# Kernel optimization log

Measured on AMD Instinct MI355X. Metric: run time of the kernel, lower is better.

## Reference

```python
import jax, jax.numpy as jnp
import numpy as np

N_GRAPHS = 16
NODES_PER = 420
N = N_GRAPHS * NODES_PER      # 6720 nodes
DEG = 8
E = N * DEG                   # 53760 edges
HEADS = 2
IN_DIM = 2048
H1 = 1024                     # conv1 out per head
H2 = 64                       # conv2 out (heads=1)
OUT_DIM = 18
SCALE = 0.02


def _lin(x, W, b):
    return x @ W + b


def _transformer_conv(x, src, dst, Wq, bq, Wk, bk, Wv, bv, Ws, bs, heads, d):
    # PyG TransformerConv: per-edge dot-product attention, softmax over incoming
    # edges of each destination node, scatter-sum of messages, + root skip.
    n = x.shape[0]
    q = _lin(x, Wq, bq).reshape(n, heads, d)
    k = _lin(x, Wk, bk).reshape(n, heads, d)
    v = _lin(x, Wv, bv).reshape(n, heads, d)
    alpha = (q[dst] * k[src]).sum(-1) / jnp.sqrt(jnp.asarray(d, x.dtype))  # [E, heads]
    amax = jax.ops.segment_max(alpha, dst, num_segments=n)
    ex = jnp.exp(alpha - amax[dst])
    denom = jax.ops.segment_sum(ex, dst, num_segments=n)
    a = ex / (denom[dst] + 1e-16)
    out = jax.ops.segment_sum(v[src] * a[..., None], dst, num_segments=n)  # [N, heads, d]
    return out.reshape(n, heads * d) + _lin(x, Ws, bs)


def setup_inputs() -> dict:
    key = jax.random.key(0)
    ks = jax.random.split(key, 32)
    x = jax.random.normal(ks[0], (N, IN_DIM), dtype=jnp.float32)
    dst = jax.random.randint(ks[1], (E,), 0, N)
    # keep edges within each 420-node graph
    src = (dst // NODES_PER) * NODES_PER + jax.random.randint(ks[2], (E,), 0, NODES_PER)
    edge_index = jnp.stack([src, dst]).astype(jnp.int64)  # [2, E]
    connectivity = jax.random.randint(ks[3], (N,), 1, 6).astype(jnp.int64)  # lobes 1..5
    p = lambda i, shape: SCALE * jax.random.normal(ks[i], shape, dtype=jnp.float32)
    inp = {
        'x': x, 'edge_index': edge_index, 'connectivity': connectivity,
        'node_pe': p(4, (NODES_PER, IN_DIM)),
        'lobe_pe': p(5, (5, IN_DIM)),
        'lung_pe': p(6, (2, IN_DIM)),
        'Wq1': p(7, (IN_DIM, HEADS * H1)), 'bq1': jnp.zeros((HEADS * H1,), jnp.float32),
        'Wk1': p(8, (IN_DIM, HEADS * H1)), 'bk1': jnp.zeros((HEADS * H1,), jnp.float32),
        'Wv1': p(9, (IN_DIM, HEADS * H1)), 'bv1': jnp.zeros((HEADS * H1,), jnp.float32),
        'Ws1': p(10, (IN_DIM, HEADS * H1)), 'bs1': jnp.zeros((HEADS * H1,), jnp.float32),
        'Wq2': p(11, (HEADS * H1, H2)), 'bq2': jnp.zeros((H2,), jnp.float32),
        'Wk2': p(12, (HEADS * H1, H2)), 'bk2': jnp.zeros((H2,), jnp.float32),
        'Wv2': p(13, (HEADS * H1, H2)), 'bv2': jnp.zeros((H2,), jnp.float32),
        'Ws2': p(14, (HEADS * H1, H2)), 'bs2': jnp.zeros((H2,), jnp.float32),
        'W_fc1': p(15, (NODES_PER * H2, 256)), 'b_fc1': jnp.zeros((256,), jnp.float32),
        'W_fc2': p(16, (256, 128)), 'b_fc2': jnp.zeros((128,), jnp.float32),
        'W_fc3': p(17, (128, 64)), 'b_fc3': jnp.zeros((64,), jnp.float32),
        'W_fc4': p(18, (64, OUT_DIM)), 'b_fc4': jnp.zeros((OUT_DIM,), jnp.float32),
    }
    return inp


def reference(x, edge_index, connectivity, node_pe, lobe_pe, lung_pe,
              Wq1, bq1, Wk1, bk1, Wv1, bv1, Ws1, bs1,
              Wq2, bq2, Wk2, bk2, Wv2, bv2, Ws2, bs2,
              W_fc1, b_fc1, W_fc2, b_fc2, W_fc3, b_fc3, W_fc4, b_fc4):
    src, dst = edge_index[0], edge_index[1]
    # positional embeddings: node PE tiled per graph, lobe PE (conn in 1..5),
    # lung PE (lobes 1,2 -> lung 0; lobes 3,4,5 -> lung 1)
    h = x + jnp.tile(node_pe, (N_GRAPHS, 1))
    h = h + lobe_pe[connectivity - 1]
    h = h + lung_pe[jnp.where(connectivity <= 2, 0, 1)]
    h = jax.nn.relu(_transformer_conv(h, src, dst, Wq1, bq1, Wk1, bk1, Wv1, bv1, Ws1, bs1, HEADS, H1))
    h = jax.nn.relu(_transformer_conv(h, src, dst, Wq2, bq2, Wk2, bk2, Wv2, bv2, Ws2, bs2, 1, H2))
    h = h.reshape(-1, NODES_PER * H2)  # [B, 420*64]
    h = jax.nn.relu(_lin(h, W_fc1, b_fc1))
    h = jax.nn.relu(_lin(h, W_fc2, b_fc2))
    h = jax.nn.relu(_lin(h, W_fc3, b_fc3))
    return _lin(h, W_fc4, b_fc4)
```

## Files before the change

kernel.cpp:

```cpp
#include <hip/hip_runtime.h>
#include <stdint.h>

#define N_GRAPHS 16
#define NODES_PER 420
#define NN (N_GRAPHS * NODES_PER)
#define MP 6784
#define EE (NN * 8)
#define IN_DIM 2048
#define NCAT1 8192
#define NCAT2 256
#define KDIM 2048

typedef __bf16 bf16x8 __attribute__((ext_vector_type(8)));
typedef float f32x4 __attribute__((ext_vector_type(4)));
typedef unsigned short u16x8 __attribute__((ext_vector_type(8)));

__device__ __forceinline__ unsigned short f2bf(float f) {
  unsigned u = __float_as_uint(f);
  u += 0x7FFFu + ((u >> 16) & 1u);
  return (unsigned short)(u >> 16);
}
__device__ __forceinline__ float bf2f(unsigned short h) {
  return __uint_as_float(((unsigned)h) << 16);
}

__device__ __forceinline__ void gl2lds16(const void* g, const void* l) {
  __builtin_amdgcn_global_load_lds(
      (const __attribute__((address_space(1))) void*)(uintptr_t)g,
      (__attribute__((address_space(3))) void*)(unsigned int)(uintptr_t)l,
      16, 0, 0);
}

__global__ void prep_k(int* cnt, float* bcat1, float* f1,
                       const float* bq1, const float* bk1, const float* bv1, const float* bs1,
                       const float* bfc1) {
  int i = blockIdx.x * 256 + threadIdx.x;
  if (i < NN) cnt[i] = 0;
  if (i < NCAT1) {
    const float* p = i < 2048 ? bq1 : i < 4096 ? bk1 : i < 6144 ? bv1 : bs1;
    bcat1[i] = p[i & 2047];
  }
  if (i < 16 * 256) f1[i] = bfc1[i & 255];
}

__global__ void cnt_edges_k(const int* __restrict__ ei, int* __restrict__ cnt) {
  int e = blockIdx.x * 256 + threadIdx.x;
  if (e < EE) atomicAdd(&cnt[ei[EE + e]], 1);
}

__global__ __launch_bounds__(64) void scan_offs_k(const int* __restrict__ cnt,
                                                  int* __restrict__ offs,
                                                  int* __restrict__ cursor) {
  const int t = threadIdx.x;
  const int base = t * 105;
  int s = 0;
#pragma unroll 1
  for (int j = 0; j < 105; j++) s += cnt[base + j];
  int pfx = s;
#pragma unroll
  for (int d = 1; d < 64; d <<= 1) {
    int v = __shfl_up(pfx, d, 64);
    if (t >= d) pfx += v;
  }
  int run = pfx - s;
#pragma unroll 1
  for (int j = 0; j < 105; j++) {
    int idx = base + j;
    offs[idx] = run; cursor[idx] = run; run += cnt[idx];
  }
  if (t == 63) offs[NN] = run;
}

__global__ void scatter_k(const int* __restrict__ ei, int* __restrict__ cursor,
                          int* __restrict__ psrc) {
  int e = blockIdx.x * 256 + threadIdx.x;
  if (e < EE) {
    int d = ei[EE + e];
    int pos = atomicAdd(&cursor[d], 1);
    psrc[pos] = ei[e];
  }
}

__global__ void pe_add_k(const float* __restrict__ x, const int* __restrict__ conn,
                         const float* __restrict__ npe, const float* __restrict__ lpe,
                         const float* __restrict__ gpe, unsigned short* __restrict__ h0,
                         float* __restrict__ qkvs2,
                         const float* __restrict__ bq2, const float* __restrict__ bk2,
                         const float* __restrict__ bv2, const float* __restrict__ bs2) {
  const int n = blockIdx.x, t = threadIdx.x;
  const int c = conn[n];
  const float4* x4 = (const float4*)(x + (size_t)n * IN_DIM);
  const float4* n4 = (const float4*)(npe + (size_t)(n % NODES_PER) * IN_DIM);
  const float4* l4 = (const float4*)(lpe + (size_t)(c - 1) * IN_DIM);
  const float4* g4 = (const float4*)(gpe + (size_t)(c <= 2 ? 0 : 1) * IN_DIM);
  ushort4* o4 = (ushort4*)(h0 + (size_t)n * IN_DIM);
#pragma unroll
  for (int i = 0; i < 2; i++) {
    int idx = i * 256 + t;
    float4 a = x4[idx], b = n4[idx], cc = l4[idx], d = g4[idx];
    ushort4 o;
    o.x = f2bf(a.x + b.x + cc.x + d.x);
    o.y = f2bf(a.y + b.y + cc.y + d.y);
    o.z = f2bf(a.z + b.z + cc.z + d.z);
    o.w = f2bf(a.w + b.w + cc.w + d.w);
    o4[idx] = o;
  }
  const float* bp = t < 64 ? bq2 : t < 128 ? bk2 : t < 192 ? bv2 : bs2;
  qkvs2[(size_t)n * NCAT2 + t] = bp[t & 63];
}

__global__ void transw_k(const float* Wq1, const float* Wk1, const float* Wv1, const float* Ws1,
                         const float* Wq2, const float* Wk2, const float* Wv2, const float* Ws2,
                         unsigned short* __restrict__ o1, unsigned short* __restrict__ o2) {
  __shared__ float tile[32][33];
  const int z = blockIdx.z;
  const float* W;
  unsigned short* o;
  int n0, Ncol;
  const int k0 = blockIdx.y * 32;
  if (z < 4) {
    W = z == 0 ? Wq1 : z == 1 ? Wk1 : z == 2 ? Wv1 : Ws1;
    o = o1 + (size_t)z * 2048 * KDIM;
    n0 = blockIdx.x * 32; Ncol = 2048;
  } else {
    if (blockIdx.x >= 8) return;
    const int m = blockIdx.x >> 1;
    W = m == 0 ? Wq2 : m == 1 ? Wk2 : m == 2 ? Wv2 : Ws2;
    o = o2 + (size_t)m * 64 * KDIM;
    n0 = (blockIdx.x & 1) * 32; Ncol = 64;
  }
  const int tx = threadIdx.x, ty = threadIdx.y;
#pragma unroll
  for (int r = 0; r < 4; r++)
    tile[ty + r * 8][tx] = W[(size_t)(k0 + ty + r * 8) * Ncol + n0 + tx];
  __syncthreads();
#pragma unroll
  for (int r = 0; r < 4; r++)
    o[(size_t)(n0 + ty + r * 8) * KDIM + k0 + tx] = f2bf(tile[tx][ty + r * 8]);
}

template <int BM, int BN, int OUTF>
__launch_bounds__(256, 3)
__global__ void gemm_bt_k(const unsigned short* __restrict__ A,
                          const unsigned short* __restrict__ Bt,
                          const float* __restrict__ bias, void* __restrict__ C,
                          int Nsz, int K, int kIters) {
  constexpr int BK = 64;
  constexpr int WTM = BM / 32, WTN = BN / 32;
  constexpr int RA = BM / 32, RB = BN / 32;
  __shared__ __align__(16) unsigned short lA[BM * BK];
  __shared__ __align__(16) unsigned short lB[BN * BK];
  const int t = threadIdx.x;
  const int w = t >> 6, lane = t & 63;
  const int wm = w >> 1, wn = w & 1;
  const int quad = lane >> 4, l16 = lane & 15;
  const int m0 = blockIdx.y * BM, n0 = blockIdx.x * BN;

  f32x4 acc[WTM][WTN];
#pragma unroll
  for (int i = 0; i < WTM; i++)
#pragma unroll
    for (int j = 0; j < WTN; j++)
#pragma unroll
      for (int r = 0; r < 4; r++) acc[i][j][r] = 0.f;

  const int srow = t >> 3;
  const int scol = ((t & 7) ^ (srow & 7)) * 8;
  const unsigned short* Ab = A + (size_t)(m0 + srow) * K + scol + blockIdx.z * (size_t)kIters * BK;
  const unsigned short* Bb = Bt + (size_t)(n0 + srow) * K + scol + blockIdx.z * (size_t)kIters * BK;

  for (int it = 0; it < kIters; it++) {
    const int k0 = it * BK;
    __syncthreads();
#pragma unroll
    for (int r = 0; r < RA; r++)
      gl2lds16(Ab + (size_t)r * 32 * K + k0, (const char*)lA + r * 4096 + t * 16);
#pragma unroll
    for (int r = 0; r < RB; r++)
      gl2lds16(Bb + (size_t)r * 32 * K + k0, (const char*)lB + r * 4096 + t * 16);
    __syncthreads();

#pragma unroll
    for (int s = 0; s < 2; s++) {
      bf16x8 afr[WTM], bfr[WTN];
#pragma unroll
      for (int i = 0; i < WTM; i++) {
        int row = wm * (BM / 2) + i * 16 + l16;
        int slot = (s * 4 + quad) ^ (row & 7);
        afr[i] = __builtin_bit_cast(bf16x8, *(const int4*)(&lA[row * 64 + slot * 8]));
      }
#pragma unroll
      for (int j = 0; j < WTN; j++) {
        int row = wn * (BN / 2) + j * 16 + l16;
        int slot = (s * 4 + quad) ^ (row & 7);
        bfr[j] = __builtin_bit_cast(bf16x8, *(const int4*)(&lB[row * 64 + slot * 8]));
      }
#pragma unroll
      for (int i = 0; i < WTM; i++)
#pragma unroll
        for (int j = 0; j < WTN; j++)
          acc[i][j] = __builtin_amdgcn_mfma_f32_16x16x32_bf16(afr[i], bfr[j], acc[i][j], 0, 0, 0);
    }
  }

#pragma unroll
  for (int j = 0; j < WTN; j++) {
    const int col = n0 + wn * (BN / 2) + j * 16 + l16;
    const float bs = OUTF ? 0.f : bias[col];
#pragma unroll
    for (int i = 0; i < WTM; i++) {
#pragma unroll
      for (int r = 0; r < 4; r++) {
        int row = m0 + wm * (BM / 2) + i * 16 + quad * 4 + r;
        if constexpr (OUTF)
          atomicAdd(&((float*)C)[(size_t)row * Nsz + col], acc[i][j][r]);
        else
          ((unsigned short*)C)[(size_t)row * Nsz + col] = f2bf(acc[i][j][r] + bs);
      }
    }
  }
}

__global__ __launch_bounds__(256) void attn1_k(const unsigned short* __restrict__ qkvs,
                                               const int* __restrict__ offs,
                                               const int* __restrict__ psrc,
                                               unsigned short* __restrict__ h1) {
  const int bid = blockIdx.x;
  const int xcd = bid & 7, idx = bid >> 3;
  const int head = idx / 840;
  const int r2 = idx - head * 840;
  const int g = xcd * 2 + r2 / 420;
  const int n = g * 420 + r2 % 420;
  const int t = threadIdx.x, w = t >> 6, lane = t & 63;
  __shared__ __align__(16) unsigned short s_q[1024];
  __shared__ float s_al[64];
  __shared__ int s_src[64];
  __shared__ float s_m, s_l, s_sc;
  const size_t base = (size_t)n * NCAT1;
  const size_t ho = (size_t)head * 1024;
  *(ushort4*)(s_q + t * 4) = *(const ushort4*)(qkvs + base + ho + t * 4);
  float acc[4] = {0.f, 0.f, 0.f, 0.f};
  if (t == 0) { s_m = -1e30f; s_l = 0.f; }
  __syncthreads();
  const int e0 = offs[n], e1 = offs[n + 1];
  for (int c0 = e0; c0 < e1; c0 += 64) {
    const int ce = min(64, e1 - c0);
    if (t < ce) s_src[t] = psrc[c0 + t];
    __syncthreads();
    for (int e = w; e < ce; e += 4) {
      const unsigned short* kp = qkvs + (size_t)s_src[e] * NCAT1 + 2048 + ho;
      float p = 0.f;
#pragma unroll
      for (int i = 0; i < 2; i++) {
        u16x8 kv = *(const u16x8*)(kp + i * 512 + lane * 8);
        u16x8 qv = *(const u16x8*)(s_q + i * 512 + lane * 8);
#pragma unroll
        for (int j = 0; j < 8; j++) p += bf2f(qv[j]) * bf2f(kv[j]);
      }
#pragma unroll
      for (int s = 32; s > 0; s >>= 1) p += __shfl_xor(p, s, 64);
      if (lane == 0) s_al[e] = p * 0.03125f;
    }
    __syncthreads();
    if (t == 0) {
      float mo = s_m, mn = mo;
      for (int e = 0; e < ce; e++) mn = fmaxf(mn, s_al[e]);
      float sc = __expf(mo - mn);
      float l = s_l * sc;
      for (int e = 0; e < ce; e++) {
        float we = __expf(s_al[e] - mn);
        l += we;
        s_al[e] = we;
      }
      s_m = mn; s_l = l; s_sc = sc;
    }
    __syncthreads();
    const float sc = s_sc;
#pragma unroll
    for (int j = 0; j < 4; j++) acc[j] *= sc;
    for (int e = 0; e < ce; e++) {
      const unsigned short* vp = qkvs + (size_t)s_src[e] * NCAT1 + 4096 + ho;
      const float we = s_al[e];
      ushort4 vv = *(const ushort4*)(vp + t * 4);
      acc[0] += we * bf2f(vv.x);
      acc[1] += we * bf2f(vv.y);
      acc[2] += we * bf2f(vv.z);
      acc[3] += we * bf2f(vv.w);
    }
    __syncthreads();
  }
  const float inv = 1.f / (s_l + 1e-16f);
  ushort4 sk = *(const ushort4*)(qkvs + base + 6144 + ho + t * 4);
  ushort4 o;
  o.x = f2bf(fmaxf(acc[0] * inv + bf2f(sk.x), 0.f));
  o.y = f2bf(fmaxf(acc[1] * inv + bf2f(sk.y), 0.f));
  o.z = f2bf(fmaxf(acc[2] * inv + bf2f(sk.z), 0.f));
  o.w = f2bf(fmaxf(acc[3] * inv + bf2f(sk.w), 0.f));
  *(ushort4*)(h1 + (size_t)n * 2048 + ho + t * 4) = o;
}

__global__ __launch_bounds__(64) void attn2_k(const float* __restrict__ qkvs2,
                                              const int* __restrict__ offs,
                                              const int* __restrict__ psrc,
                                              float* __restrict__ h2) {
  const int bid = blockIdx.x;
  const int xcd = bid & 7, idx = bid >> 3;
  const int g = xcd * 2 + idx / 420;
  const int n = g * 420 + idx % 420;
  const int t = threadIdx.x;
  const size_t rb = (size_t)n * NCAT2;
  const float q = qkvs2[rb + t];
  float m = -1e30f, l = 0.f, acc = 0.f;
  const int e0 = offs[n], e1 = offs[n + 1];
  for (int e = e0; e < e1; e++) {
    const int src = psrc[e];
    float p = q * qkvs2[(size_t)src * NCAT2 + 64 + t];
#pragma unroll
    for (int s = 32; s > 0; s >>= 1) p += __shfl_xor(p, s, 64);
    p *= 0.125f;
    const float mn = fmaxf(m, p);
    const float sc = __expf(m - mn), we = __expf(p - mn);
    const float v = qkvs2[(size_t)src * NCAT2 + 128 + t];
    l = l * sc + we;
    acc = acc * sc + we * v;
    m = mn;
  }
  float o = acc / (l + 1e-16f) + qkvs2[rb + 192 + t];
  h2[(size_t)n * 64 + t] = fmaxf(o, 0.f);
}

__global__ __launch_bounds__(256) void fc1_k(const float* __restrict__ h2,
                                             const float* __restrict__ W,
                                             float* __restrict__ f1) {
  __shared__ float sA[16][256];
  const int t = threadIdx.x, k0 = blockIdx.x * 256;
#pragma unroll
  for (int r = 0; r < 16; r++) sA[r][t] = h2[(size_t)r * 26880 + k0 + t];
  __syncthreads();
  float acc[16];
#pragma unroll
  for (int r = 0; r < 16; r++) acc[r] = 0.f;
  for (int kk = 0; kk < 256; kk++) {
    const float wv = W[(size_t)(k0 + kk) * 256 + t];
#pragma unroll
    for (int r = 0; r < 16; r++) acc[r] += sA[r][kk] * wv;
  }
#pragma unroll
  for (int r = 0; r < 16; r++) atomicAdd(&f1[r * 256 + t], acc[r]);
}

__global__ __launch_bounds__(128) void fc234_k(const float* __restrict__ f1,
                                               const float* __restrict__ W2, const float* __restrict__ b2,
                                               const float* __restrict__ W3, const float* __restrict__ b3,
                                               const float* __restrict__ W4, const float* __restrict__ b4,
                                               float* __restrict__ out) {
  const int row = blockIdx.x, t = threadIdx.x;
  __shared__ float s2[128], s3[64];
  float acc = 0.f;
  for (int k = 0; k < 256; k++) acc += fmaxf(f1[row * 256 + k], 0.f) * W2[k * 128 + t];
  s2[t] = fmaxf(acc + b2[t], 0.f);
  __syncthreads();
  if (t < 64) {
    float a3 = 0.f;
    for (int k = 0; k < 128; k++) a3 += s2[k] * W3[k * 64 + t];
    s3[t] = fmaxf(a3 + b3[t], 0.f);
  }
  __syncthreads();
  if (t < 18) {
    float a4 = 0.f;
    for (int k = 0; k < 64; k++) a4 += s3[k] * W4[k * 18 + t];
    out[row * 18 + t] = a4 + b4[t];
  }
}

extern "C" void kernel_launch(void* const* d_in, const int* in_sizes, int n_in,
                              void* d_out, int out_size, void* d_ws, size_t ws_size,
                              hipStream_t stream) {
  const float* x    = (const float*)d_in[0];
  const int*   ei   = (const int*)d_in[1];
  const int*   conn = (const int*)d_in[2];
  const float* npe  = (const float*)d_in[3];
  const float* lpe  = (const float*)d_in[4];
  const float* gpe  = (const float*)d_in[5];
  const float* Wq1 = (const float*)d_in[6];  const float* bq1 = (const float*)d_in[7];
  const float* Wk1 = (const float*)d_in[8];  const float* bk1 = (const float*)d_in[9];
  const float* Wv1 = (const float*)d_in[10]; const float* bv1 = (const float*)d_in[11];
  const float* Ws1 = (const float*)d_in[12]; const float* bs1 = (const float*)d_in[13];
  const float* Wq2 = (const float*)d_in[14]; const float* bq2 = (const float*)d_in[15];
  const float* Wk2 = (const float*)d_in[16]; const float* bk2 = (const float*)d_in[17];
  const float* Wv2 = (const float*)d_in[18]; const float* bv2 = (const float*)d_in[19];
  const float* Ws2 = (const float*)d_in[20]; const float* bs2 = (const float*)d_in[21];
  const float* Wf1 = (const float*)d_in[22]; const float* bf1 = (const float*)d_in[23];
  const float* Wf2 = (const float*)d_in[24]; const float* bf2 = (const float*)d_in[25];
  const float* Wf3 = (const float*)d_in[26]; const float* bf3 = (const float*)d_in[27];
  const float* Wf4 = (const float*)d_in[28]; const float* bf4 = (const float*)d_in[29];
  float* out = (float*)d_out;

  char* ws = (char*)d_ws;
  size_t off = 0;
  auto alloc = [&](size_t bytes) -> void* {
    void* p = ws + off;
    off += (bytes + 255) & ~(size_t)255;
    return p;
  };
  unsigned short* h0    = (unsigned short*)alloc((size_t)MP * IN_DIM * 2);
  unsigned short* w1t   = (unsigned short*)alloc((size_t)NCAT1 * KDIM * 2);
  unsigned short* qkvs1 = (unsigned short*)alloc((size_t)MP * NCAT1 * 2);
  unsigned short* w2t   = (unsigned short*)alloc((size_t)NCAT2 * KDIM * 2);
  float* qkvs2 = (float*)alloc((size_t)MP * NCAT2 * 4);
  float* h2    = (float*)alloc((size_t)NN * 64 * 4);
  float* bcat1 = (float*)alloc(NCAT1 * 4);
  float* f1    = (float*)alloc(16 * 256 * 4);
  int* cnt    = (int*)alloc(NN * 4);
  int* offs   = (int*)alloc((NN + 1) * 4);
  int* cursor = (int*)alloc(NN * 4);
  int* psrc   = (int*)alloc(EE * 4);
  unsigned short* h1 = w1t;

  prep_k<<<32, 256, 0, stream>>>(cnt, bcat1, f1, bq1, bk1, bv1, bs1, bf1);
  cnt_edges_k<<<EE / 256, 256, 0, stream>>>(ei, cnt);
  scan_offs_k<<<1, 64, 0, stream>>>(cnt, offs, cursor);
  scatter_k<<<EE / 256, 256, 0, stream>>>(ei, cursor, psrc);
  pe_add_k<<<NN, 256, 0, stream>>>(x, conn, npe, lpe, gpe, h0, qkvs2,
                                   bq2, bk2, bv2, bs2);
  transw_k<<<dim3(64, 64, 5), dim3(32, 8), 0, stream>>>(
      Wq1, Wk1, Wv1, Ws1, Wq2, Wk2, Wv2, Ws2, w1t, w2t);
  gemm_bt_k<128, 128, 0><<<dim3(NCAT1 / 128, MP / 128, 1), 256, 0, stream>>>(
      h0, w1t, bcat1, qkvs1, NCAT1, KDIM, KDIM / 64);
  attn1_k<<<2 * NN, 256, 0, stream>>>(qkvs1, offs, psrc, h1);
  gemm_bt_k<64, 64, 1><<<dim3(NCAT2 / 64, MP / 64, 4), 256, 0, stream>>>(
      h1, w2t, nullptr, qkvs2, NCAT2, KDIM, KDIM / 64 / 4);
  attn2_k<<<NN, 64, 0, stream>>>(qkvs2, offs, psrc, h2);
  fc1_k<<<26880 / 256, 256, 0, stream>>>(h2, Wf1, f1);
  fc234_k<<<16, 128, 0, stream>>>(f1, Wf2, bf2, Wf3, bf3, Wf4, bf4, out);
}
```

Baseline: 613.9 us.

## Replace split-K atomics with partial buffers plus combine, parallelize scan, tweak GEMM occupancy

The conv2 split-K GEMM now writes each K-slice to its own partial buffer, reusing h0, with nontemporal stores instead of float atomicAdd. A new combine kernel sums the four slices and adds the conv2 bias, which moves out of pe_add_k into prep_k. The single-block offset scan widens from 64 to 256 threads with register caching and a cross-wave prefix, and the GEMM launch bounds ask for 4 blocks per SM instead of 3. This removes atomic contention at the cost of an extra kernel launch and more memory traffic, and the higher occupancy target may force register spills in the large GEMM.

```diff
diff --git a/kernel.cpp b/kernel.cpp
--- a/kernel.cpp
+++ b/kernel.cpp
@@ -31,8 +31,9 @@
       16, 0, 0);
 }
 
-__global__ void prep_k(int* cnt, float* bcat1, float* f1,
+__global__ void prep_k(int* cnt, float* bcat1, float* bcat2, float* f1,
                        const float* bq1, const float* bk1, const float* bv1, const float* bs1,
+                       const float* bq2, const float* bk2, const float* bv2, const float* bs2,
                        const float* bfc1) {
   int i = blockIdx.x * 256 + threadIdx.x;
   if (i < NN) cnt[i] = 0;
@@ -40,6 +41,10 @@
     const float* p = i < 2048 ? bq1 : i < 4096 ? bk1 : i < 6144 ? bv1 : bs1;
     bcat1[i] = p[i & 2047];
   }
+  if (i < NCAT2) {
+    const float* p = i < 64 ? bq2 : i < 128 ? bk2 : i < 192 ? bv2 : bs2;
+    bcat2[i] = p[i & 63];
+  }
   if (i < 16 * 256) f1[i] = bfc1[i & 255];
 }
 
@@ -48,27 +53,41 @@
   if (e < EE) atomicAdd(&cnt[ei[EE + e]], 1);
 }
 
-__global__ __launch_bounds__(64) void scan_offs_k(const int* __restrict__ cnt,
-                                                  int* __restrict__ offs,
-                                                  int* __restrict__ cursor) {
+__global__ __launch_bounds__(256) void scan_offs_k(const int* __restrict__ cnt,
+                                                   int* __restrict__ offs,
+                                                   int* __restrict__ cursor) {
   const int t = threadIdx.x;
-  const int base = t * 105;
+  const int base = t * 27;
+  int c[27];
   int s = 0;
-#pragma unroll 1
-  for (int j = 0; j < 105; j++) s += cnt[base + j];
+#pragma unroll
+  for (int j = 0; j < 27; j++) {
+    int idx = base + j;
+    c[j] = idx < NN ? cnt[idx] : 0;
+    s += c[j];
+  }
+  const int lane = t & 63, w = t >> 6;
   int pfx = s;
 #pragma unroll
   for (int d = 1; d < 64; d <<= 1) {
     int v = __shfl_up(pfx, d, 64);
-    if (t >= d) pfx += v;
-  }
-  int run = pfx - s;
-#pragma unroll 1
-  for (int j = 0; j < 105; j++) {
+    if (lane >= d) pfx += v;
+  }
+  __shared__ int wtot[4];
+  if (lane == 63) wtot[w] = pfx;
+  __syncthreads();
+  int add = 0;
+#pragma unroll
+  for (int i = 0; i < 4; i++)
+    if (i < w) add += wtot[i];
+  int run = add + pfx - s;
+#pragma unroll
+  for (int j = 0; j < 27; j++) {
     int idx = base + j;
-    offs[idx] = run; cursor[idx] = run; run += cnt[idx];
-  }
-  if (t == 63) offs[NN] = run;
+    if (idx < NN) { offs[idx] = run; cursor[idx] = run; }
+    run += c[j];
+  }
+  if (t == 255) offs[NN] = add + pfx;
 }
 
 __global__ void scatter_k(const int* __restrict__ ei, int* __restrict__ cursor,
@@ -83,10 +102,7 @@
 
 __global__ void pe_add_k(const float* __restrict__ x, const int* __restrict__ conn,
                          const float* __restrict__ npe, const float* __restrict__ lpe,
-                         const float* __restrict__ gpe, unsigned short* __restrict__ h0,
-                         float* __restrict__ qkvs2,
-                         const float* __restrict__ bq2, const float* __restrict__ bk2,
-                         const float* __restrict__ bv2, const float* __restrict__ bs2) {
+                         const float* __restrict__ gpe, unsigned short* __restrict__ h0) {
   const int n = blockIdx.x, t = threadIdx.x;
   const int c = conn[n];
   const float4* x4 = (const float4*)(x + (size_t)n * IN_DIM);
@@ -105,8 +121,6 @@
     o.w = f2bf(a.w + b.w + cc.w + d.w);
     o4[idx] = o;
   }
-  const float* bp = t < 64 ? bq2 : t < 128 ? bk2 : t < 192 ? bv2 : bs2;
-  qkvs2[(size_t)n * NCAT2 + t] = bp[t & 63];
 }
 
 __global__ void transw_k(const float* Wq1, const float* Wk1, const float* Wv1, const float* Ws1,
@@ -140,7 +154,7 @@
 }
 
 template <int BM, int BN, int OUTF>
-__launch_bounds__(256, 3)
+__launch_bounds__(256, 4)
 __global__ void gemm_bt_k(const unsigned short* __restrict__ A,
                           const unsigned short* __restrict__ Bt,
                           const float* __restrict__ bias, void* __restrict__ C,
@@ -212,13 +226,32 @@
 #pragma unroll
       for (int r = 0; r < 4; r++) {
         int row = m0 + wm * (BM / 2) + i * 16 + quad * 4 + r;
-        if constexpr (OUTF)
-          atomicAdd(&((float*)C)[(size_t)row * Nsz + col], acc[i][j][r]);
-        else
-          ((unsigned short*)C)[(size_t)row * Nsz + col] = f2bf(acc[i][j][r] + bs);
+        if constexpr (OUTF) {
+          float* p = (float*)C + (size_t)blockIdx.z * MP * Nsz + (size_t)row * Nsz + col;
+          __builtin_nontemporal_store(acc[i][j][r], p);
+        } else {
+          unsigned short* p = (unsigned short*)C + (size_t)row * Nsz + col;
+          __builtin_nontemporal_store(f2bf(acc[i][j][r] + bs), p);
+        }
       }
     }
   }
+}
+
+__global__ void combine2_k(const float* __restrict__ part, const float* __restrict__ bcat2,
+                           float* __restrict__ qkvs2) {
+  const int i = blockIdx.x * 256 + threadIdx.x;
+  const float4 a = ((const float4*)part)[i];
+  const float4 b = ((const float4*)(part + (size_t)MP * NCAT2))[i];
+  const float4 c = ((const float4*)(part + (size_t)2 * MP * NCAT2))[i];
+  const float4 d = ((const float4*)(part + (size_t)3 * MP * NCAT2))[i];
+  const float4 bs = ((const float4*)bcat2)[i & 63];
+  float4 o;
+  o.x = a.x + b.x + c.x + d.x + bs.x;
+  o.y = a.y + b.y + c.y + d.y + bs.y;
+  o.z = a.z + b.z + c.z + d.z + bs.z;
+  o.w = a.w + b.w + c.w + d.w + bs.w;
+  ((float4*)qkvs2)[i] = o;
 }
 
 __global__ __launch_bounds__(256) void attn1_k(const unsigned short* __restrict__ qkvs,
@@ -410,26 +443,29 @@
   float* qkvs2 = (float*)alloc((size_t)MP * NCAT2 * 4);
   float* h2    = (float*)alloc((size_t)NN * 64 * 4);
   float* bcat1 = (float*)alloc(NCAT1 * 4);
+  float* bcat2 = (float*)alloc(NCAT2 * 4);
   float* f1    = (float*)alloc(16 * 256 * 4);
   int* cnt    = (int*)alloc(NN * 4);
   int* offs   = (int*)alloc((NN + 1) * 4);
   int* cursor = (int*)alloc(NN * 4);
   int* psrc   = (int*)alloc(EE * 4);
   unsigned short* h1 = w1t;
-
-  prep_k<<<32, 256, 0, stream>>>(cnt, bcat1, f1, bq1, bk1, bv1, bs1, bf1);
+  float* part2 = (float*)h0;
+
+  prep_k<<<32, 256, 0, stream>>>(cnt, bcat1, bcat2, f1,
+                                 bq1, bk1, bv1, bs1, bq2, bk2, bv2, bs2, bf1);
   cnt_edges_k<<<EE / 256, 256, 0, stream>>>(ei, cnt);
-  scan_offs_k<<<1, 64, 0, stream>>>(cnt, offs, cursor);
+  scan_offs_k<<<1, 256, 0, stream>>>(cnt, offs, cursor);
   scatter_k<<<EE / 256, 256, 0, stream>>>(ei, cursor, psrc);
-  pe_add_k<<<NN, 256, 0, stream>>>(x, conn, npe, lpe, gpe, h0, qkvs2,
-                                   bq2, bk2, bv2, bs2);
+  pe_add_k<<<NN, 256, 0, stream>>>(x, conn, npe, lpe, gpe, h0);
   transw_k<<<dim3(64, 64, 5), dim3(32, 8), 0, stream>>>(
       Wq1, Wk1, Wv1, Ws1, Wq2, Wk2, Wv2, Ws2, w1t, w2t);
   gemm_bt_k<128, 128, 0><<<dim3(NCAT1 / 128, MP / 128, 1), 256, 0, stream>>>(
       h0, w1t, bcat1, qkvs1, NCAT1, KDIM, KDIM / 64);
   attn1_k<<<2 * NN, 256, 0, stream>>>(qkvs1, offs, psrc, h1);
   gemm_bt_k<64, 64, 1><<<dim3(NCAT2 / 64, MP / 64, 4), 256, 0, stream>>>(
-      h1, w2t, nullptr, qkvs2, NCAT2, KDIM, KDIM / 64 / 4);
+      h1, w2t, nullptr, part2, NCAT2, KDIM, KDIM / 64 / 4);
+  combine2_k<<<MP / 4, 256, 0, stream>>>(part2, bcat2, qkvs2);
   attn2_k<<<NN, 64, 0, stream>>>(qkvs2, offs, psrc, h2);
   fc1_k<<<26880 / 256, 256, 0, stream>>>(h2, Wf1, f1);
   fc234_k<<<16, 128, 0, stream>>>(f1, Wf2, bf2, Wf3, bf3, Wf4, bf4, out);
```

Result: slower. 633.5 us (+3.2%).
